# Performance work log

Hardware: AMD Instinct MI355X
Metric: run time of the kernel (lower is better)

Reference implementation:

```python
import jax, jax.numpy as jnp
import numpy as np

B, S, D, E, K = 4, 4096, 2048, 64, 2


def setup_inputs() -> dict:
    key = jax.random.key(0)
    k1, k2 = jax.random.split(key)
    hidden_states = jax.random.normal(k1, (B, S, D), dtype=jnp.float32)
    gate_weight = jax.random.normal(k2, (E, D), dtype=jnp.float32) * 0.02
    return {"hidden_states": hidden_states, "gate_weight": gate_weight}


def reference(hidden_states, gate_weight):
    b, s, d = hidden_states.shape
    e = gate_weight.shape[0]
    n = b * s
    x = hidden_states.reshape(n, d)
    logits = x @ gate_weight.T                                  # [N, E]
    # Original reassigns gate_logits = softmax(gate_logits) in fp32.
    probs = jax.nn.softmax(logits.astype(jnp.float32), axis=-1)  # [N, E]

    top_v, top_i = jax.lax.top_k(probs, K)                       # [N, K]
    top_k_gates = top_v  # normalize_gate_prob_before_dropping=False

    oh = jax.nn.one_hot(top_i, e, dtype=probs.dtype)             # [N, K, E]
    gates = jnp.einsum('nke,nk->ne', oh, top_k_gates)            # scatter of top-k gates

    # Auxiliary losses (training path, use_aux_loss=True)
    gates_mean = gates.mean(axis=0)                              # [E]
    selection_mean = oh.sum(axis=(0, 1)) / n                     # [E]
    load_balancing_loss = (gates_mean * selection_mean).sum() * e
    # NOTE: original computes z-loss on the softmaxed probs (gate_logits was overwritten)
    router_z_loss = (jax.nn.logsumexp(probs, axis=-1) ** 2).mean()

    # torch scatter_ with index [B,S,1,1] only ever writes slot k=0.
    dispatch0 = oh.sum(axis=1).reshape(b, s, e)                  # 1.0 at top-k experts
    combine0 = gates.reshape(b, s, e)
    pad = ((0, 0), (0, 0), (0, 0), (0, K - 1))
    dispatch_tensor = jnp.pad(dispatch0[..., None], pad)         # [B,S,E,K]
    combine_tensor = jnp.pad(combine0[..., None], pad)           # [B,S,E,K]

    return dispatch_tensor, combine_tensor, load_balancing_loss, router_z_loss
```

## Files before the change

kernel.cpp:

```cpp
#include <hip/hip_runtime.h>
#include <hip/hip_bf16.h>
#include <cstddef>

namespace {
constexpr int kD = 2048;
constexpr int kE = 64;
constexpr int kN = 16384;
constexpr size_t kDispatchFloats = (size_t)kN * kE * 2;
constexpr size_t kWsplitOff = 1024;
}

typedef short short8_t __attribute__((ext_vector_type(8)));
typedef float f32x4 __attribute__((ext_vector_type(4)));

__global__ void zero_ws_kernel(float* __restrict__ ws) {
  ws[threadIdx.x] = 0.0f;
}

__device__ __forceinline__ void split3(float f, unsigned short& s1,
                                       unsigned short& s2, unsigned short& s3) {
  __hip_bfloat16 h1 = __float2bfloat16(f);
  float r1 = (f - __bfloat162float(h1)) * 256.0f;
  __hip_bfloat16 h2 = __float2bfloat16(r1);
  float r2 = (r1 - __bfloat162float(h2)) * 256.0f;
  __hip_bfloat16 h3 = __float2bfloat16(r2);
  s1 = __builtin_bit_cast(unsigned short, h1);
  s2 = __builtin_bit_cast(unsigned short, h2);
  s3 = __builtin_bit_cast(unsigned short, h3);
}

__global__ __launch_bounds__(256)
void split_w_kernel(const float* __restrict__ W, unsigned short* __restrict__ img) {
  const int t   = blockIdx.x * 256 + threadIdx.x;
  const int dq  = t >> 12;
  const int c   = (t >> 9) & 7;
  const int row = (t >> 3) & 63;
  const int cs8 = t & 7;
  const int co  = cs8 ^ (row & 7);
  const float* src = W + (size_t)row * kD + dq * 512 + c * 64 + co * 8;
  const float4 v0 = *reinterpret_cast<const float4*>(src);
  const float4 v1 = *reinterpret_cast<const float4*>(src + 4);
  short8_t o1, o2, o3;
  unsigned short s1, s2, s3;
  split3(v0.x, s1, s2, s3); o1[0]=(short)s1; o2[0]=(short)s2; o3[0]=(short)s3;
  split3(v0.y, s1, s2, s3); o1[1]=(short)s1; o2[1]=(short)s2; o3[1]=(short)s3;
  split3(v0.z, s1, s2, s3); o1[2]=(short)s1; o2[2]=(short)s2; o3[2]=(short)s3;
  split3(v0.w, s1, s2, s3); o1[3]=(short)s1; o2[3]=(short)s2; o3[3]=(short)s3;
  split3(v1.x, s1, s2, s3); o1[4]=(short)s1; o2[4]=(short)s2; o3[4]=(short)s3;
  split3(v1.y, s1, s2, s3); o1[5]=(short)s1; o2[5]=(short)s2; o3[5]=(short)s3;
  split3(v1.z, s1, s2, s3); o1[6]=(short)s1; o2[6]=(short)s2; o3[6]=(short)s3;
  split3(v1.w, s1, s2, s3); o1[7]=(short)s1; o2[7]=(short)s2; o3[7]=(short)s3;
  unsigned short* dst = img + (size_t)(dq * 8 + c) * 12288 + row * 64 + cs8 * 8;
  *reinterpret_cast<short8_t*>(dst + 0 * 4096) = o1;
  *reinterpret_cast<short8_t*>(dst + 1 * 4096) = o2;
  *reinterpret_cast<short8_t*>(dst + 2 * 4096) = o3;
}

__device__ __forceinline__ void conv_store4(float4 f0, float4 f1, float4 f2,
                                            float4 f3,
                                            unsigned short (*dst)[64][64],
                                            int srow, int seg) {
  const float4 v[4] = {f0, f1, f2, f3};
  short8_t o1[2], o2[2], o3[2];
#pragma unroll
  for (int j = 0; j < 4; ++j) {
    const float4 f = v[j];
    const int ch = j >> 1, b0 = (j & 1) * 4;
    unsigned short s1, s2, s3;
    split3(f.x, s1, s2, s3); o1[ch][b0+0]=(short)s1; o2[ch][b0+0]=(short)s2; o3[ch][b0+0]=(short)s3;
    split3(f.y, s1, s2, s3); o1[ch][b0+1]=(short)s1; o2[ch][b0+1]=(short)s2; o3[ch][b0+1]=(short)s3;
    split3(f.z, s1, s2, s3); o1[ch][b0+2]=(short)s1; o2[ch][b0+2]=(short)s2; o3[ch][b0+2]=(short)s3;
    split3(f.w, s1, s2, s3); o1[ch][b0+3]=(short)s1; o2[ch][b0+3]=(short)s2; o3[ch][b0+3]=(short)s3;
  }
#pragma unroll
  for (int ch = 0; ch < 2; ++ch) {
    const int col = (seg * 2 + ch) ^ (srow & 7);
    *reinterpret_cast<short8_t*>(&dst[0][srow][col * 8]) = o1[ch];
    *reinterpret_cast<short8_t*>(&dst[1][srow][col * 8]) = o2[ch];
    *reinterpret_cast<short8_t*>(&dst[2][srow][col * 8]) = o3[ch];
  }
}

__global__ __launch_bounds__(256)
void logits_kernel(const float* __restrict__ x,
                   const unsigned short* __restrict__ wimg,
                   float* __restrict__ out) {
  __shared__ unsigned short xs[3][64][64];
  __shared__ unsigned short wt[3][64][64];

  const int tid  = threadIdx.x;
  const int lane = tid & 63;
  const int wv   = __builtin_amdgcn_readfirstlane(tid >> 6);
  const int wr   = wv >> 1;
  const int wc   = wv & 1;
  const int tile = blockIdx.x & 255;
  const int dq   = blockIdx.x >> 8;
  const int lrow = lane & 15;
  const int lk   = lane >> 4;

  const int row = tid >> 2, seg = tid & 3;
  const float4* __restrict__ bx = reinterpret_cast<const float4*>(x) +
      ((size_t)tile * 64 + row) * 512 + dq * 128 + seg * 4;
  const unsigned short* __restrict__ wbase =
      wimg + (size_t)dq * 8 * 12288 + tid * 8;
  unsigned short* wtf = &wt[0][0][0];

  f32x4 acc0[2][2], acc1[2][2], acc2[2][2];
  const f32x4 z4 = {0.0f, 0.0f, 0.0f, 0.0f};
#pragma unroll
  for (int a = 0; a < 2; ++a)
#pragma unroll
    for (int b = 0; b < 2; ++b) { acc0[a][b] = z4; acc1[a][b] = z4; acc2[a][b] = z4; }

  float4 vx0 = bx[0], vx1 = bx[1], vx2 = bx[2], vx3 = bx[3];

  for (int c = 0; c < 8; ++c) {
    const unsigned short* wsrc = wbase + (size_t)c * 12288;
#pragma unroll
    for (int i = 0; i < 6; ++i)
      __builtin_amdgcn_global_load_lds(
          (const __attribute__((address_space(1))) void*)(wsrc + i * 2048),
          (__attribute__((address_space(3))) void*)(wtf + i * 2048 + wv * 512),
          16, 0, 0);
    __builtin_amdgcn_sched_barrier(0);
    const float4 xa = vx0, xb = vx1, xc2 = vx2, xd = vx3;
    const int cn = (c + 1) & 7;
    vx0 = bx[cn * 16 + 0]; vx1 = bx[cn * 16 + 1];
    vx2 = bx[cn * 16 + 2]; vx3 = bx[cn * 16 + 3];
    conv_store4(xa, xb, xc2, xd, xs, row, seg);
    asm volatile("s_waitcnt vmcnt(4) lgkmcnt(0)" ::: "memory");
    __builtin_amdgcn_sched_barrier(0);
    __builtin_amdgcn_s_barrier();
    __builtin_amdgcn_sched_barrier(0);
#pragma unroll
    for (int ks = 0; ks < 2; ++ks) {
      const int kc = ks * 4 + lk;
      short8_t a1[2], a2[2], a3[2], b1[2], b2[2], b3[2];
#pragma unroll
      for (int nt = 0; nt < 2; ++nt) {
        const int e = wc * 32 + nt * 16 + lrow;
        const int cw = (kc ^ (e & 7)) * 8;
        b1[nt] = *reinterpret_cast<const short8_t*>(&wt[0][e][cw]);
        b2[nt] = *reinterpret_cast<const short8_t*>(&wt[1][e][cw]);
        b3[nt] = *reinterpret_cast<const short8_t*>(&wt[2][e][cw]);
      }
#pragma unroll
      for (int mt = 0; mt < 2; ++mt) {
        const int r = wr * 32 + mt * 16 + lrow;
        const int cw = (kc ^ (r & 7)) * 8;
        a1[mt] = *reinterpret_cast<const short8_t*>(&xs[0][r][cw]);
        a2[mt] = *reinterpret_cast<const short8_t*>(&xs[1][r][cw]);
        a3[mt] = *reinterpret_cast<const short8_t*>(&xs[2][r][cw]);
      }
#pragma unroll
      for (int mt = 0; mt < 2; ++mt)
#pragma unroll
        for (int nt = 0; nt < 2; ++nt) {
          acc0[mt][nt] = __builtin_amdgcn_mfma_f32_16x16x32_bf16(a1[mt], b1[nt], acc0[mt][nt], 0, 0, 0);
          acc1[mt][nt] = __builtin_amdgcn_mfma_f32_16x16x32_bf16(a1[mt], b2[nt], acc1[mt][nt], 0, 0, 0);
          acc1[mt][nt] = __builtin_amdgcn_mfma_f32_16x16x32_bf16(a2[mt], b1[nt], acc1[mt][nt], 0, 0, 0);
          acc2[mt][nt] = __builtin_amdgcn_mfma_f32_16x16x32_bf16(a1[mt], b3[nt], acc2[mt][nt], 0, 0, 0);
          acc2[mt][nt] = __builtin_amdgcn_mfma_f32_16x16x32_bf16(a3[mt], b1[nt], acc2[mt][nt], 0, 0, 0);
          acc2[mt][nt] = __builtin_amdgcn_mfma_f32_16x16x32_bf16(a2[mt], b2[nt], acc2[mt][nt], 0, 0, 0);
        }
    }
    __builtin_amdgcn_sched_barrier(0);
    __builtin_amdgcn_s_barrier();
  }

  const float k8 = 1.0f / 256.0f, k16 = 1.0f / 65536.0f;
  float* __restrict__ base = out + ((dq < 2) ? (size_t)0 : kDispatchFloats);
#pragma unroll
  for (int mt = 0; mt < 2; ++mt)
#pragma unroll
    for (int r = 0; r < 4; ++r) {
      const int trow = wr * 32 + mt * 16 + lk * 4 + r;
      const size_t n = (size_t)tile * 64 + trow;
      float* __restrict__ dst =
          base + n * 128 + (dq & 1) * 64 + wc * 32 + lrow;
#pragma unroll
      for (int nt = 0; nt < 2; ++nt)
        dst[nt * 16] = acc0[mt][nt][r] + acc1[mt][nt][r] * k8 + acc2[mt][nt][r] * k16;
    }
}

__global__ __launch_bounds__(256)
void gate_kernel(float* __restrict__ out, float* __restrict__ ws) {
  __shared__ float lg[64][65];
  __shared__ int ti0[64], ti1[64];
  __shared__ float tv0[64], tv1[64], tz2[64];
  const int tid  = threadIdx.x;
  const int tile = blockIdx.x;

  float* __restrict__ outd = out + (size_t)tile * 8192;
  float* __restrict__ outc = out + kDispatchFloats + (size_t)tile * 8192;
  const float4* __restrict__ d4 = reinterpret_cast<const float4*>(outd);
  const float4* __restrict__ c4 = reinterpret_cast<const float4*>(outc);

  const int tq = tid >> 4, q = tid & 15;
#pragma unroll
  for (int k = 0; k < 4; ++k) {
    const int t = k * 16 + tq;
    const float4 a = d4[t * 32 + q];
    const float4 b = d4[t * 32 + 16 + q];
    const float4 c = c4[t * 32 + q];
    const float4 d = c4[t * 32 + 16 + q];
    lg[t][q * 4 + 0] = a.x + b.x + c.x + d.x;
    lg[t][q * 4 + 1] = a.y + b.y + c.y + d.y;
    lg[t][q * 4 + 2] = a.z + b.z + c.z + d.z;
    lg[t][q * 4 + 3] = a.w + b.w + c.w + d.w;
  }
  __syncthreads();

  if (tid < 64) {
    float v0 = -INFINITY, v1 = -INFINITY;
    int i0 = 0, i1 = 0;
    for (int e = 0; e < kE; ++e) {
      const float l = lg[tid][e];
      if (l > v0) { v1 = v0; i1 = i0; v0 = l; i0 = e; }
      else if (l > v1) { v1 = l; i1 = e; }
    }
    const float m = v0;
    float s = 0.0f;
    for (int e = 0; e < kE; ++e) s += __expf(lg[tid][e] - m);
    const float rs = 1.0f / s;
    float zexp = 0.0f;
    for (int e = 0; e < kE; ++e) zexp += __expf(__expf(lg[tid][e] - m) * rs);
    const float z = logf(zexp);
    ti0[tid] = i0; ti1[tid] = i1;
    tv0[tid] = rs;
    tv1[tid] = __expf(v1 - m) * rs;
    tz2[tid] = z * z;
  }
  __syncthreads();

  if (tid < kE) {
    float g = 0.0f, cnt = 0.0f;
    for (int t = 0; t < 64; ++t) {
      if (ti0[t] == tid) { g += tv0[t]; cnt += 1.0f; }
      if (ti1[t] == tid) { g += tv1[t]; cnt += 1.0f; }
    }
    atomicAdd(&ws[tid], g);
    atomicAdd(&ws[kE + tid], cnt);
    float z2 = tz2[tid];
    for (int off = 32; off; off >>= 1) z2 += __shfl_down(z2, off);
    if (tid == 0) atomicAdd(&ws[2 * kE], z2);
  }

  {
    const int t = tid >> 2, sub = tid & 3;
    const int i0 = ti0[t], i1 = ti1[t];
    const float v0 = tv0[t], v1 = tv1[t];
    float4* __restrict__ dp = reinterpret_cast<float4*>(outd) + t * 32;
    float4* __restrict__ cp = reinterpret_cast<float4*>(outc) + t * 32;
#pragma unroll
    for (int j = 0; j < 8; ++j) {
      const int qq = sub * 8 + j;
      const int e0 = qq * 2, e1 = qq * 2 + 1;
      const float d0v = (e0 == i0 || e0 == i1) ? 1.0f : 0.0f;
      const float d1v = (e1 == i0 || e1 == i1) ? 1.0f : 0.0f;
      const float c0 = (e0 == i0) ? v0 : ((e0 == i1) ? v1 : 0.0f);
      const float c1 = (e1 == i0) ? v0 : ((e1 == i1) ? v1 : 0.0f);
      dp[qq] = make_float4(d0v, 0.0f, d1v, 0.0f);
      cp[qq] = make_float4(c0, 0.0f, c1, 0.0f);
    }
  }
}

__global__ void finalize_kernel(const float* __restrict__ ws,
                                float* __restrict__ out) {
  const int e = threadIdx.x;
  float prod = ws[e] * ws[kE + e];
  for (int off = 32; off; off >>= 1) prod += __shfl_down(prod, off);
  if (e == 0) {
    const size_t base = kDispatchFloats * 2;
    const float invN = 1.0f / (float)kN;
    out[base]     = prod * ((float)kE * invN * invN);
    out[base + 1] = ws[2 * kE] * invN;
  }
}

extern "C" void kernel_launch(void* const* d_in, const int* in_sizes, int n_in,
                              void* d_out, int out_size, void* d_ws,
                              size_t ws_size, hipStream_t stream) {
  const float* x = (const float*)d_in[0];
  const float* W = (const float*)d_in[1];
  float* out = (float*)d_out;
  float* ws = (float*)d_ws;
  unsigned short* wimg = (unsigned short*)(ws + kWsplitOff);

  zero_ws_kernel<<<1, 256, 0, stream>>>(ws);
  split_w_kernel<<<64, 256, 0, stream>>>(W, wimg);
  logits_kernel<<<1024, 256, 0, stream>>>(x, wimg, out);
  gate_kernel<<<256, 256, 0, stream>>>(out, ws);
  finalize_kernel<<<1, kE, 0, stream>>>(ws, out);
}
```

Measured before the change: 79.38 us.

## Split K across two wave groups in logits kernel with LDS reduction

Doubles the logits block from 256 to 512 threads. The two halves of each K chunk go to separate wave groups (kh), and each thread now converts and stores half as many x values. At the end, the partial accumulators from the kh=1 waves go through LDS, reusing the xs buffer, and the kh=0 waves add them before the global write. The aim is more waves in flight to hide global-load and conversion latency. The cost is an extra LDS reduction and barrier, and possibly lower occupancy per CU.

```diff
diff --git a/kernel.cpp b/kernel.cpp
--- a/kernel.cpp
+++ b/kernel.cpp
@@ -56,32 +56,26 @@
   *reinterpret_cast<short8_t*>(dst + 2 * 4096) = o3;
 }
 
-__device__ __forceinline__ void conv_store4(float4 f0, float4 f1, float4 f2,
-                                            float4 f3,
+__device__ __forceinline__ void conv_store8(float4 a, float4 b,
                                             unsigned short (*dst)[64][64],
-                                            int srow, int seg) {
-  const float4 v[4] = {f0, f1, f2, f3};
-  short8_t o1[2], o2[2], o3[2];
-#pragma unroll
-  for (int j = 0; j < 4; ++j) {
-    const float4 f = v[j];
-    const int ch = j >> 1, b0 = (j & 1) * 4;
-    unsigned short s1, s2, s3;
-    split3(f.x, s1, s2, s3); o1[ch][b0+0]=(short)s1; o2[ch][b0+0]=(short)s2; o3[ch][b0+0]=(short)s3;
-    split3(f.y, s1, s2, s3); o1[ch][b0+1]=(short)s1; o2[ch][b0+1]=(short)s2; o3[ch][b0+1]=(short)s3;
-    split3(f.z, s1, s2, s3); o1[ch][b0+2]=(short)s1; o2[ch][b0+2]=(short)s2; o3[ch][b0+2]=(short)s3;
-    split3(f.w, s1, s2, s3); o1[ch][b0+3]=(short)s1; o2[ch][b0+3]=(short)s2; o3[ch][b0+3]=(short)s3;
-  }
-#pragma unroll
-  for (int ch = 0; ch < 2; ++ch) {
-    const int col = (seg * 2 + ch) ^ (srow & 7);
-    *reinterpret_cast<short8_t*>(&dst[0][srow][col * 8]) = o1[ch];
-    *reinterpret_cast<short8_t*>(&dst[1][srow][col * 8]) = o2[ch];
-    *reinterpret_cast<short8_t*>(&dst[2][srow][col * 8]) = o3[ch];
-  }
-}
-
-__global__ __launch_bounds__(256)
+                                            int row, int seg) {
+  short8_t o1, o2, o3;
+  unsigned short s1, s2, s3;
+  split3(a.x, s1, s2, s3); o1[0]=(short)s1; o2[0]=(short)s2; o3[0]=(short)s3;
+  split3(a.y, s1, s2, s3); o1[1]=(short)s1; o2[1]=(short)s2; o3[1]=(short)s3;
+  split3(a.z, s1, s2, s3); o1[2]=(short)s1; o2[2]=(short)s2; o3[2]=(short)s3;
+  split3(a.w, s1, s2, s3); o1[3]=(short)s1; o2[3]=(short)s2; o3[3]=(short)s3;
+  split3(b.x, s1, s2, s3); o1[4]=(short)s1; o2[4]=(short)s2; o3[4]=(short)s3;
+  split3(b.y, s1, s2, s3); o1[5]=(short)s1; o2[5]=(short)s2; o3[5]=(short)s3;
+  split3(b.z, s1, s2, s3); o1[6]=(short)s1; o2[6]=(short)s2; o3[6]=(short)s3;
+  split3(b.w, s1, s2, s3); o1[7]=(short)s1; o2[7]=(short)s2; o3[7]=(short)s3;
+  const int col = seg ^ (row & 7);
+  *reinterpret_cast<short8_t*>(&dst[0][row][col * 8]) = o1;
+  *reinterpret_cast<short8_t*>(&dst[1][row][col * 8]) = o2;
+  *reinterpret_cast<short8_t*>(&dst[2][row][col * 8]) = o3;
+}
+
+__global__ __launch_bounds__(512)
 void logits_kernel(const float* __restrict__ x,
                    const unsigned short* __restrict__ wimg,
                    float* __restrict__ out) {
@@ -91,16 +85,17 @@
   const int tid  = threadIdx.x;
   const int lane = tid & 63;
   const int wv   = __builtin_amdgcn_readfirstlane(tid >> 6);
-  const int wr   = wv >> 1;
-  const int wc   = wv & 1;
+  const int wr   = wv >> 2;
+  const int wc   = (wv >> 1) & 1;
+  const int kh   = wv & 1;
   const int tile = blockIdx.x & 255;
   const int dq   = blockIdx.x >> 8;
   const int lrow = lane & 15;
   const int lk   = lane >> 4;
 
-  const int row = tid >> 2, seg = tid & 3;
+  const int row = tid >> 3, seg = tid & 7;
   const float4* __restrict__ bx = reinterpret_cast<const float4*>(x) +
-      ((size_t)tile * 64 + row) * 512 + dq * 128 + seg * 4;
+      ((size_t)tile * 64 + row) * 512 + dq * 128 + seg * 2;
   const unsigned short* __restrict__ wbase =
       wimg + (size_t)dq * 8 * 12288 + tid * 8;
   unsigned short* wtf = &wt[0][0][0];
@@ -112,29 +107,28 @@
 #pragma unroll
     for (int b = 0; b < 2; ++b) { acc0[a][b] = z4; acc1[a][b] = z4; acc2[a][b] = z4; }
 
-  float4 vx0 = bx[0], vx1 = bx[1], vx2 = bx[2], vx3 = bx[3];
+  float4 vx0 = bx[0], vx1 = bx[1];
 
   for (int c = 0; c < 8; ++c) {
     const unsigned short* wsrc = wbase + (size_t)c * 12288;
 #pragma unroll
-    for (int i = 0; i < 6; ++i)
+    for (int i = 0; i < 3; ++i)
       __builtin_amdgcn_global_load_lds(
-          (const __attribute__((address_space(1))) void*)(wsrc + i * 2048),
-          (__attribute__((address_space(3))) void*)(wtf + i * 2048 + wv * 512),
+          (const __attribute__((address_space(1))) void*)(wsrc + i * 4096),
+          (__attribute__((address_space(3))) void*)(wtf + i * 4096 + wv * 512),
           16, 0, 0);
     __builtin_amdgcn_sched_barrier(0);
-    const float4 xa = vx0, xb = vx1, xc2 = vx2, xd = vx3;
+    const float4 xa = vx0, xb = vx1;
     const int cn = (c + 1) & 7;
-    vx0 = bx[cn * 16 + 0]; vx1 = bx[cn * 16 + 1];
-    vx2 = bx[cn * 16 + 2]; vx3 = bx[cn * 16 + 3];
-    conv_store4(xa, xb, xc2, xd, xs, row, seg);
-    asm volatile("s_waitcnt vmcnt(4) lgkmcnt(0)" ::: "memory");
+    vx0 = bx[cn * 16 + 0];
+    vx1 = bx[cn * 16 + 1];
+    conv_store8(xa, xb, xs, row, seg);
+    asm volatile("s_waitcnt vmcnt(2) lgkmcnt(0)" ::: "memory");
     __builtin_amdgcn_sched_barrier(0);
     __builtin_amdgcn_s_barrier();
     __builtin_amdgcn_sched_barrier(0);
-#pragma unroll
-    for (int ks = 0; ks < 2; ++ks) {
-      const int kc = ks * 4 + lk;
+    {
+      const int kc = kh * 4 + lk;
       short8_t a1[2], a2[2], a3[2], b1[2], b2[2], b3[2];
 #pragma unroll
       for (int nt = 0; nt < 2; ++nt) {
@@ -169,19 +163,39 @@
   }
 
   const float k8 = 1.0f / 256.0f, k16 = 1.0f / 65536.0f;
-  float* __restrict__ base = out + ((dq < 2) ? (size_t)0 : kDispatchFloats);
-#pragma unroll
-  for (int mt = 0; mt < 2; ++mt)
-#pragma unroll
-    for (int r = 0; r < 4; ++r) {
-      const int trow = wr * 32 + mt * 16 + lk * 4 + r;
-      const size_t n = (size_t)tile * 64 + trow;
-      float* __restrict__ dst =
-          base + n * 128 + (dq & 1) * 64 + wc * 32 + lrow;
+  float* __restrict__ mbuf = reinterpret_cast<float*>(&xs[0][0][0]);
+  if (kh == 1) {
+#pragma unroll
+    for (int mt = 0; mt < 2; ++mt)
 #pragma unroll
       for (int nt = 0; nt < 2; ++nt)
-        dst[nt * 16] = acc0[mt][nt][r] + acc1[mt][nt][r] * k8 + acc2[mt][nt][r] * k16;
-    }
+#pragma unroll
+        for (int r = 0; r < 4; ++r) {
+          const int trow = wr * 32 + mt * 16 + lk * 4 + r;
+          const int col  = wc * 32 + nt * 16 + lrow;
+          mbuf[trow * 65 + col] =
+              acc0[mt][nt][r] + acc1[mt][nt][r] * k8 + acc2[mt][nt][r] * k16;
+        }
+  }
+  __syncthreads();
+  if (kh == 0) {
+    float* __restrict__ base = out + ((dq < 2) ? (size_t)0 : kDispatchFloats);
+#pragma unroll
+    for (int mt = 0; mt < 2; ++mt)
+#pragma unroll
+      for (int r = 0; r < 4; ++r) {
+        const int trow = wr * 32 + mt * 16 + lk * 4 + r;
+        const size_t n = (size_t)tile * 64 + trow;
+        float* __restrict__ dst =
+            base + n * 128 + (dq & 1) * 64 + wc * 32 + lrow;
+#pragma unroll
+        for (int nt = 0; nt < 2; ++nt) {
+          const int col = wc * 32 + nt * 16 + lrow;
+          dst[nt * 16] = acc0[mt][nt][r] + acc1[mt][nt][r] * k8 +
+                         acc2[mt][nt][r] * k16 + mbuf[trow * 65 + col];
+        }
+      }
+  }
 }
 
 __global__ __launch_bounds__(256)
@@ -291,7 +305,7 @@
 
   zero_ws_kernel<<<1, 256, 0, stream>>>(ws);
   split_w_kernel<<<64, 256, 0, stream>>>(W, wimg);
-  logits_kernel<<<1024, 256, 0, stream>>>(x, wimg, out);
+  logits_kernel<<<1024, 512, 0, stream>>>(x, wimg, out);
   gate_kernel<<<256, 256, 0, stream>>>(out, ws);
   finalize_kernel<<<1, kE, 0, stream>>>(ws, out);
 }
```

Measured after the change: 73.29 us. 7.7% less time.

## Load x straight into MFMA registers and double-buffer weight tiles in LDS

Applied to the files above, without the earlier changes.

The activation tile no longer passes through LDS. Each lane loads the fp32 x values it needs directly from global memory in MFMA operand layout and splits them into three bf16 parts in registers. The weight image is now double-buffered in LDS, with the next chunk prefetched asynchronously while the current one is consumed. A register-prefetch copy is kept for x. This removes the LDS writes and reads for x and one barrier's worth of exposure, and adds an occupancy hint of 3 blocks. In exchange, x loads are less coalesced (16-byte strided row reads), each x element is split redundantly by both column waves, and register pressure rises.

```diff
diff --git a/kernel.cpp b/kernel.cpp
--- a/kernel.cpp
+++ b/kernel.cpp
@@ -27,6 +27,16 @@
   s1 = __builtin_bit_cast(unsigned short, h1);
   s2 = __builtin_bit_cast(unsigned short, h2);
   s3 = __builtin_bit_cast(unsigned short, h3);
+}
+
+__device__ __forceinline__ void split8(f32x4 a, f32x4 b, short8_t& o1,
+                                       short8_t& o2, short8_t& o3) {
+  unsigned short s1, s2, s3;
+#define SP(v, i, j) \
+  split3((v)[i], s1, s2, s3); o1[j]=(short)s1; o2[j]=(short)s2; o3[j]=(short)s3;
+  SP(a, 0, 0) SP(a, 1, 1) SP(a, 2, 2) SP(a, 3, 3)
+  SP(b, 0, 4) SP(b, 1, 5) SP(b, 2, 6) SP(b, 3, 7)
+#undef SP
 }
 
 __global__ __launch_bounds__(256)
@@ -56,37 +66,11 @@
   *reinterpret_cast<short8_t*>(dst + 2 * 4096) = o3;
 }
 
-__device__ __forceinline__ void conv_store4(float4 f0, float4 f1, float4 f2,
-                                            float4 f3,
-                                            unsigned short (*dst)[64][64],
-                                            int srow, int seg) {
-  const float4 v[4] = {f0, f1, f2, f3};
-  short8_t o1[2], o2[2], o3[2];
-#pragma unroll
-  for (int j = 0; j < 4; ++j) {
-    const float4 f = v[j];
-    const int ch = j >> 1, b0 = (j & 1) * 4;
-    unsigned short s1, s2, s3;
-    split3(f.x, s1, s2, s3); o1[ch][b0+0]=(short)s1; o2[ch][b0+0]=(short)s2; o3[ch][b0+0]=(short)s3;
-    split3(f.y, s1, s2, s3); o1[ch][b0+1]=(short)s1; o2[ch][b0+1]=(short)s2; o3[ch][b0+1]=(short)s3;
-    split3(f.z, s1, s2, s3); o1[ch][b0+2]=(short)s1; o2[ch][b0+2]=(short)s2; o3[ch][b0+2]=(short)s3;
-    split3(f.w, s1, s2, s3); o1[ch][b0+3]=(short)s1; o2[ch][b0+3]=(short)s2; o3[ch][b0+3]=(short)s3;
-  }
-#pragma unroll
-  for (int ch = 0; ch < 2; ++ch) {
-    const int col = (seg * 2 + ch) ^ (srow & 7);
-    *reinterpret_cast<short8_t*>(&dst[0][srow][col * 8]) = o1[ch];
-    *reinterpret_cast<short8_t*>(&dst[1][srow][col * 8]) = o2[ch];
-    *reinterpret_cast<short8_t*>(&dst[2][srow][col * 8]) = o3[ch];
-  }
-}
-
-__global__ __launch_bounds__(256)
+__global__ __launch_bounds__(256, 3)
 void logits_kernel(const float* __restrict__ x,
                    const unsigned short* __restrict__ wimg,
                    float* __restrict__ out) {
-  __shared__ unsigned short xs[3][64][64];
-  __shared__ unsigned short wt[3][64][64];
+  __shared__ unsigned short wt[2][3][64][64];
 
   const int tid  = threadIdx.x;
   const int lane = tid & 63;
@@ -98,12 +82,12 @@
   const int lrow = lane & 15;
   const int lk   = lane >> 4;
 
-  const int row = tid >> 2, seg = tid & 3;
-  const float4* __restrict__ bx = reinterpret_cast<const float4*>(x) +
-      ((size_t)tile * 64 + row) * 512 + dq * 128 + seg * 4;
+  const float* __restrict__ xb[2];
+  xb[0] = x + (size_t)(tile * 64 + wr * 32 + lrow) * kD + dq * 512 + lk * 8;
+  xb[1] = xb[0] + (size_t)16 * kD;
+
   const unsigned short* __restrict__ wbase =
       wimg + (size_t)dq * 8 * 12288 + tid * 8;
-  unsigned short* wtf = &wt[0][0][0];
 
   f32x4 acc0[2][2], acc1[2][2], acc2[2][2];
   const f32x4 z4 = {0.0f, 0.0f, 0.0f, 0.0f};
@@ -112,60 +96,83 @@
 #pragma unroll
     for (int b = 0; b < 2; ++b) { acc0[a][b] = z4; acc1[a][b] = z4; acc2[a][b] = z4; }
 
-  float4 vx0 = bx[0], vx1 = bx[1], vx2 = bx[2], vx3 = bx[3];
-
-  for (int c = 0; c < 8; ++c) {
-    const unsigned short* wsrc = wbase + (size_t)c * 12288;
+  f32x4 xc[8], xn[8];
+
+  {
+    unsigned short* dst = &wt[0][0][0][0];
 #pragma unroll
     for (int i = 0; i < 6; ++i)
       __builtin_amdgcn_global_load_lds(
-          (const __attribute__((address_space(1))) void*)(wsrc + i * 2048),
-          (__attribute__((address_space(3))) void*)(wtf + i * 2048 + wv * 512),
+          (const __attribute__((address_space(1))) void*)(wbase + i * 2048),
+          (__attribute__((address_space(3))) void*)(dst + i * 2048 + wv * 512),
           16, 0, 0);
+#pragma unroll
+    for (int mt = 0; mt < 2; ++mt)
+#pragma unroll
+      for (int ks = 0; ks < 2; ++ks)
+#pragma unroll
+        for (int j = 0; j < 2; ++j)
+          xc[mt * 4 + ks * 2 + j] =
+              *reinterpret_cast<const f32x4*>(xb[mt] + ks * 32 + j * 4);
     __builtin_amdgcn_sched_barrier(0);
-    const float4 xa = vx0, xb = vx1, xc2 = vx2, xd = vx3;
-    const int cn = (c + 1) & 7;
-    vx0 = bx[cn * 16 + 0]; vx1 = bx[cn * 16 + 1];
-    vx2 = bx[cn * 16 + 2]; vx3 = bx[cn * 16 + 3];
-    conv_store4(xa, xb, xc2, xd, xs, row, seg);
-    asm volatile("s_waitcnt vmcnt(4) lgkmcnt(0)" ::: "memory");
-    __builtin_amdgcn_sched_barrier(0);
+    asm volatile("s_waitcnt vmcnt(8)" ::: "memory");
     __builtin_amdgcn_s_barrier();
+  }
+
+#pragma unroll 2
+  for (int c = 0; c < 8; ++c) {
+    const int cb = c & 1, cn = (c + 1) & 7;
+    {
+      unsigned short* dst = &wt[cb ^ 1][0][0][0];
+      const unsigned short* src = wbase + (size_t)cn * 12288;
+#pragma unroll
+      for (int i = 0; i < 6; ++i)
+        __builtin_amdgcn_global_load_lds(
+            (const __attribute__((address_space(1))) void*)(src + i * 2048),
+            (__attribute__((address_space(3))) void*)(dst + i * 2048 + wv * 512),
+            16, 0, 0);
+    }
+#pragma unroll
+    for (int mt = 0; mt < 2; ++mt)
+#pragma unroll
+      for (int ks = 0; ks < 2; ++ks)
+#pragma unroll
+        for (int j = 0; j < 2; ++j)
+          xn[mt * 4 + ks * 2 + j] = *reinterpret_cast<const f32x4*>(
+              xb[mt] + cn * 64 + ks * 32 + j * 4);
     __builtin_amdgcn_sched_barrier(0);
 #pragma unroll
     for (int ks = 0; ks < 2; ++ks) {
       const int kc = ks * 4 + lk;
-      short8_t a1[2], a2[2], a3[2], b1[2], b2[2], b3[2];
+      short8_t b1[2], b2[2], b3[2];
 #pragma unroll
       for (int nt = 0; nt < 2; ++nt) {
         const int e = wc * 32 + nt * 16 + lrow;
         const int cw = (kc ^ (e & 7)) * 8;
-        b1[nt] = *reinterpret_cast<const short8_t*>(&wt[0][e][cw]);
-        b2[nt] = *reinterpret_cast<const short8_t*>(&wt[1][e][cw]);
-        b3[nt] = *reinterpret_cast<const short8_t*>(&wt[2][e][cw]);
+        b1[nt] = *reinterpret_cast<const short8_t*>(&wt[cb][0][e][cw]);
+        b2[nt] = *reinterpret_cast<const short8_t*>(&wt[cb][1][e][cw]);
+        b3[nt] = *reinterpret_cast<const short8_t*>(&wt[cb][2][e][cw]);
       }
 #pragma unroll
       for (int mt = 0; mt < 2; ++mt) {
-        const int r = wr * 32 + mt * 16 + lrow;
-        const int cw = (kc ^ (r & 7)) * 8;
-        a1[mt] = *reinterpret_cast<const short8_t*>(&xs[0][r][cw]);
-        a2[mt] = *reinterpret_cast<const short8_t*>(&xs[1][r][cw]);
-        a3[mt] = *reinterpret_cast<const short8_t*>(&xs[2][r][cw]);
+        short8_t a1, a2, a3;
+        split8(xc[mt * 4 + ks * 2], xc[mt * 4 + ks * 2 + 1], a1, a2, a3);
+#pragma unroll
+        for (int nt = 0; nt < 2; ++nt) {
+          acc0[mt][nt] = __builtin_amdgcn_mfma_f32_16x16x32_bf16(a1, b1[nt], acc0[mt][nt], 0, 0, 0);
+          acc1[mt][nt] = __builtin_amdgcn_mfma_f32_16x16x32_bf16(a1, b2[nt], acc1[mt][nt], 0, 0, 0);
+          acc1[mt][nt] = __builtin_amdgcn_mfma_f32_16x16x32_bf16(a2, b1[nt], acc1[mt][nt], 0, 0, 0);
+          acc2[mt][nt] = __builtin_amdgcn_mfma_f32_16x16x32_bf16(a1, b3[nt], acc2[mt][nt], 0, 0, 0);
+          acc2[mt][nt] = __builtin_amdgcn_mfma_f32_16x16x32_bf16(a3, b1[nt], acc2[mt][nt], 0, 0, 0);
+          acc2[mt][nt] = __builtin_amdgcn_mfma_f32_16x16x32_bf16(a2, b2[nt], acc2[mt][nt], 0, 0, 0);
+        }
       }
-#pragma unroll
-      for (int mt = 0; mt < 2; ++mt)
-#pragma unroll
-        for (int nt = 0; nt < 2; ++nt) {
-          acc0[mt][nt] = __builtin_amdgcn_mfma_f32_16x16x32_bf16(a1[mt], b1[nt], acc0[mt][nt], 0, 0, 0);
-          acc1[mt][nt] = __builtin_amdgcn_mfma_f32_16x16x32_bf16(a1[mt], b2[nt], acc1[mt][nt], 0, 0, 0);
-          acc1[mt][nt] = __builtin_amdgcn_mfma_f32_16x16x32_bf16(a2[mt], b1[nt], acc1[mt][nt], 0, 0, 0);
-          acc2[mt][nt] = __builtin_amdgcn_mfma_f32_16x16x32_bf16(a1[mt], b3[nt], acc2[mt][nt], 0, 0, 0);
-          acc2[mt][nt] = __builtin_amdgcn_mfma_f32_16x16x32_bf16(a3[mt], b1[nt], acc2[mt][nt], 0, 0, 0);
-          acc2[mt][nt] = __builtin_amdgcn_mfma_f32_16x16x32_bf16(a2[mt], b2[nt], acc2[mt][nt], 0, 0, 0);
-        }
     }
     __builtin_amdgcn_sched_barrier(0);
+    asm volatile("s_waitcnt vmcnt(8)" ::: "memory");
     __builtin_amdgcn_s_barrier();
+#pragma unroll
+    for (int i = 0; i < 8; ++i) xc[i] = xn[i];
   }
 
   const float k8 = 1.0f / 256.0f, k16 = 1.0f / 65536.0f;
```

Result: slower. 85.62 us (+7.9%).
